# Performance work log

Measured on AMD Instinct MI355X. Metric: run time of the kernel, lower is better.

## Reference

```python
import jax, jax.numpy as jnp
import numpy as np

B, T, I, H, C, S = 512, 128, 512, 512, 97, 26  # batch, enc_len, input, hidden, classes, num_steps


def setup_inputs() -> dict:
    key = jax.random.key(0)
    ks = jax.random.split(key, 12)
    s = 0.05
    d = {}
    d["batch_H"] = jax.random.normal(ks[0], (B, T, I), dtype=jnp.float32)
    d["text"] = jax.random.randint(ks[1], (B, S), 0, C)
    # attention cell params
    d["W_feat"] = jax.random.normal(ks[2], (H, I), dtype=jnp.float32) * s   # feature_projection (no bias)
    d["W_hid"] = jax.random.normal(ks[3], (H, H), dtype=jnp.float32) * s    # hidden_projection
    d["b_hid"] = jnp.zeros((H,), dtype=jnp.float32)
    d["w_score"] = jax.random.normal(ks[4], (H,), dtype=jnp.float32) * s    # attention_score (Linear(H,1), no bias)
    # LSTMCell params, PyTorch gate order [i, f, g, o]
    d["W_ih"] = jax.random.normal(ks[5], (4 * H, I + C), dtype=jnp.float32) * s
    d["W_hh"] = jax.random.normal(ks[6], (4 * H, H), dtype=jnp.float32) * s
    d["b_ih"] = jnp.zeros((4 * H,), dtype=jnp.float32)
    d["b_hh"] = jnp.zeros((4 * H,), dtype=jnp.float32)
    # generator
    d["W_gen"] = jax.random.normal(ks[7], (C, H), dtype=jnp.float32) * s
    d["b_gen"] = jnp.zeros((C,), dtype=jnp.float32)
    return d


def reference(batch_H, text, W_feat, W_hid, b_hid, w_score, W_ih, W_hh, b_ih, b_hh, W_gen, b_gen):
    Bb, Tt, _ = batch_H.shape
    Hh = W_hid.shape[0]
    Cc = W_gen.shape[0]
    # step-invariant: project encoder features once  [B, T, H]
    feat = jnp.einsum('bti,hi->bth', batch_H, W_feat)
    onehots = jax.nn.one_hot(text, Cc, dtype=batch_H.dtype)  # [B, S, C]

    def step(carry, oh):
        h, c = carry
        hp = h @ W_hid.T + b_hid                                     # [B, H]
        e = jnp.einsum('bth,h->bt', jnp.tanh(feat + hp[:, None, :]), w_score)
        alpha = jax.nn.softmax(e, axis=1)                            # [B, T]
        ctx = jnp.einsum('bt,bti->bi', alpha, batch_H)               # [B, I]
        x = jnp.concatenate([ctx, oh], axis=1)                       # [B, I+C]
        gates = x @ W_ih.T + b_ih + h @ W_hh.T + b_hh                # [B, 4H]
        i_g, f_g, g_g, o_g = jnp.split(gates, 4, axis=1)
        c2 = jax.nn.sigmoid(f_g) * c + jax.nn.sigmoid(i_g) * jnp.tanh(g_g)
        h2 = jax.nn.sigmoid(o_g) * jnp.tanh(c2)
        return (h2, c2), h2

    init = (jnp.zeros((Bb, Hh), dtype=batch_H.dtype), jnp.zeros((Bb, Hh), dtype=batch_H.dtype))
    _, hs = jax.lax.scan(step, init, jnp.swapaxes(onehots, 0, 1))    # hs: [S, B, H]
    out_h = jnp.swapaxes(hs, 0, 1)                                   # [B, S, H]
    probs = out_h @ W_gen.T + b_gen                                  # [B, S, C]
    return probs
```

## Files before the change

### kernel.cpp

```cpp
#include <hip/hip_runtime.h>
#include <hip/hip_bf16.h>
#include <stdint.h>
#include <stddef.h>

typedef __bf16 bf16;
typedef __bf16 v8bf __attribute__((ext_vector_type(8)));
typedef float  v4f  __attribute__((ext_vector_type(4)));

#define B_ 512
#define T_ 128
#define I_ 512
#define H_ 512
#define C_ 97
#define S_ 26

__device__ __forceinline__ void async_copy16(void* lds, const void* g) {
  __builtin_amdgcn_global_load_lds((__attribute__((address_space(1))) void*)g,
                                   (__attribute__((address_space(3))) void*)lds,
                                   16, 0, 0);
}

__device__ __forceinline__ float fast_tanh(float x) {
  float e = __expf(2.0f * x);
  return fmaf(-2.0f, __builtin_amdgcn_rcpf(e + 1.0f), 1.0f);
}
__device__ __forceinline__ float fast_sigmoid(float x) {
  float t = __expf(-x);
  return __builtin_amdgcn_rcpf(1.0f + t);
}

__device__ __forceinline__ void zero_acc(v4f acc[4][4]) {
  v4f z = {0.f, 0.f, 0.f, 0.f};
#pragma unroll
  for (int i = 0; i < 4; ++i)
#pragma unroll
    for (int j = 0; j < 4; ++j) acc[i][j] = z;
}

#define WAITBAR(N)                                             \
  do {                                                         \
    asm volatile("s_waitcnt vmcnt(" #N ")" ::: "memory");      \
    __builtin_amdgcn_s_barrier();                              \
    __builtin_amdgcn_sched_barrier(0);                         \
  } while (0)

template <int KTOT>
__device__ __forceinline__ void mm_qb32(const bf16* aRow0, const bf16* aRow1,
                                        const bf16* bRow0, const bf16* bRow1,
                                        bf16* As, bf16* Bs, int tid,
                                        v4f acc[4][4]) {
  constexpr int NT = KTOT / 32;
  const int wave = tid >> 6, lane = tid & 63;
  const int wr = (wave >> 1) * 64, wc = (wave & 1) * 64;
  const int fr = lane & 15, fq = lane >> 4;
  const int s0 = tid * 8;
  const int aB = (wr + fr) * 32 + fq * 8;
  const int bB = (wc + fr) * 32 + fq * 8;
#define STG32(bi, kk)                                   \
  do {                                                  \
    const int o = (bi) * 4096 + s0;                     \
    async_copy16(As + o, aRow0 + (kk));                 \
    async_copy16(As + o + 2048, aRow1 + (kk));          \
    async_copy16(Bs + o, bRow0 + (kk));                 \
    async_copy16(Bs + o + 2048, bRow1 + (kk));          \
  } while (0)
  STG32(0, 0);
  STG32(1, 32);
  for (int t = 0; t < NT; ++t) {
    if (t + 2 < NT) {
      STG32((t + 2) & 3, (t + 2) * 32);
      WAITBAR(8);
    } else if (t + 1 < NT) {
      WAITBAR(4);
    } else {
      WAITBAR(0);
    }
    const int cb = (t & 3) * 4096;
    v8bf av[4], bv[4];
#pragma unroll
    for (int i = 0; i < 4; ++i) av[i] = *(const v8bf*)(As + cb + aB + i * 512);
#pragma unroll
    for (int j = 0; j < 4; ++j) bv[j] = *(const v8bf*)(Bs + cb + bB + j * 512);
#pragma unroll
    for (int i = 0; i < 4; ++i) {
#pragma unroll
      for (int j = 0; j < 4; ++j) {
        acc[i][j] = __builtin_amdgcn_mfma_f32_16x16x32_bf16(av[i], bv[j], acc[i][j], 0, 0, 0);
      }
    }
  }
#undef STG32
}

template <int KTOT>
__device__ __forceinline__ void mm_reg_f32a(const float* aR0, const float* aR1,
                                            const bf16* bRow0, const bf16* bRow1,
                                            bf16* As, bf16* Bs, int tid,
                                            v4f acc[4][4]) {
  const int wave = tid >> 6, lane = tid & 63;
  const int wr = (wave >> 1) * 64, wc = (wave & 1) * 64;
  const int fr = lane & 15, fq = lane >> 4;
  bf16* a_s0 = As + tid * 8;
  bf16* a_s1 = As + (tid + 256) * 8;
  bf16* b_s0 = Bs + tid * 8;
  bf16* b_s1 = Bs + (tid + 256) * 8;
  const bf16* aF[4];
  const bf16* bF[4];
#pragma unroll
  for (int i = 0; i < 4; ++i) {
    aF[i] = As + (wr + i * 16 + fr) * 32 + fq * 8;
    bF[i] = Bs + (wc + i * 16 + fr) * 32 + fq * 8;
  }
  for (int kk = 0; kk < KTOT; kk += 32) {
    v8bf va0, va1;
    const float* p0 = aR0 + kk;
    const float* p1 = aR1 + kk;
    v4f f00 = ((const v4f*)p0)[0], f01 = ((const v4f*)p0)[1];
    v4f f10 = ((const v4f*)p1)[0], f11 = ((const v4f*)p1)[1];
#pragma unroll
    for (int j = 0; j < 4; ++j) {
      va0[j] = (bf16)f00[j]; va0[j + 4] = (bf16)f01[j];
      va1[j] = (bf16)f10[j]; va1[j + 4] = (bf16)f11[j];
    }
    v8bf vb0 = *(const v8bf*)(bRow0 + kk);
    v8bf vb1 = *(const v8bf*)(bRow1 + kk);
    __syncthreads();
    *(v8bf*)a_s0 = va0;
    *(v8bf*)a_s1 = va1;
    *(v8bf*)b_s0 = vb0;
    *(v8bf*)b_s1 = vb1;
    __syncthreads();
    v8bf av[4], bv[4];
#pragma unroll
    for (int i = 0; i < 4; ++i) av[i] = *(const v8bf*)aF[i];
#pragma unroll
    for (int j = 0; j < 4; ++j) bv[j] = *(const v8bf*)bF[j];
#pragma unroll
    for (int i = 0; i < 4; ++i) {
#pragma unroll
      for (int j = 0; j < 4; ++j) {
        acc[i][j] = __builtin_amdgcn_mfma_f32_16x16x32_bf16(av[i], bv[j], acc[i][j], 0, 0, 0);
      }
    }
  }
  __syncthreads();
}

__global__ void k_cvt(const float* __restrict__ src, bf16* __restrict__ dst, int n) {
  int i = (blockIdx.x * 256 + threadIdx.x) * 4;
  if (i + 3 < n) {
    v4f f = *(const v4f*)(src + i);
#pragma unroll
    for (int j = 0; j < 4; ++j) dst[i + j] = (bf16)f[j];
  }
}

__global__ void k_repack(const float* __restrict__ Wih, const float* __restrict__ Whh,
                         bf16* __restrict__ Wcat) {
  int n = blockIdx.x;
  int t = threadIdx.x;
#pragma unroll
  for (int j = 0; j < 4; ++j) {
    int k = t * 4 + j;
    float v = (k < 512) ? Wih[(size_t)n * 609 + k] : Whh[(size_t)n * 512 + (k - 512)];
    Wcat[(size_t)n * 1024 + k] = (bf16)v;
  }
}

__global__ void k_prep_gen(const float* __restrict__ Wg, bf16* __restrict__ Wgen16) {
  int row = blockIdx.x;
  int t = threadIdx.x;
#pragma unroll
  for (int j = 0; j < 2; ++j) {
    int k = t * 2 + j;
    float v = (row < C_) ? Wg[(size_t)row * 512 + k] : 0.0f;
    Wgen16[(size_t)row * 512 + k] = (bf16)v;
  }
}

__global__ void k_prep_oht(const float* __restrict__ Wih, float* __restrict__ OHT) {
  int n = blockIdx.x * 256 + threadIdx.x;
  const float* src = Wih + (size_t)n * 609 + 512;
  for (int c = 0; c < C_; ++c) OHT[(size_t)c * 2048 + n] = src[c];
}


__global__ __launch_bounds__(256, 2) void k_feat16(const bf16* __restrict__ A,
                                                   const bf16* __restrict__ Bw,
                                                   bf16* __restrict__ F) {
  __shared__ bf16 As[4 * 4096];
  __shared__ bf16 Bs[4 * 4096];
  const int tid = threadIdx.x;
  const int m0 = blockIdx.x * 128, n0 = blockIdx.y * 128;
  const int r0 = tid >> 2, k0 = (tid & 3) * 8;
  const bf16* aRow0 = A + (size_t)(m0 + r0) * 512 + k0;
  const bf16* aRow1 = A + (size_t)(m0 + r0 + 64) * 512 + k0;
  const bf16* bRow0 = Bw + (size_t)(n0 + r0) * 512 + k0;
  const bf16* bRow1 = Bw + (size_t)(n0 + r0 + 64) * 512 + k0;
  v4f acc[4][4];
  zero_acc(acc);
  mm_qb32<512>(aRow0, aRow1, bRow0, bRow1, As, Bs, tid, acc);
  const int wave = tid >> 6, lane = tid & 63;
  const int wr = (wave >> 1) * 64, wc = (wave & 1) * 64;
  const int fr = lane & 15, fq = lane >> 4;
#pragma unroll
  for (int i = 0; i < 4; ++i) {
#pragma unroll
    for (int j = 0; j < 4; ++j) {
      int col = n0 + wc + j * 16 + fr;
#pragma unroll
      for (int r = 0; r < 4; ++r) {
        int row = m0 + wr + i * 16 + fq * 4 + r;
        F[(size_t)row * 512 + col] = (bf16)acc[i][j][r];
      }
    }
  }
}

__global__ __launch_bounds__(256, 2) void k_feat32(const float* __restrict__ A,
                                                   const bf16* __restrict__ Bw,
                                                   bf16* __restrict__ F) {
  __shared__ bf16 As[128 * 32];
  __shared__ bf16 Bs[128 * 32];
  const int tid = threadIdx.x;
  const int m0 = blockIdx.x * 128, n0 = blockIdx.y * 128;
  const int r0 = tid >> 2, k0 = (tid & 3) * 8;
  const float* aRow0 = A + (size_t)(m0 + r0) * 512 + k0;
  const float* aRow1 = A + (size_t)(m0 + r0 + 64) * 512 + k0;
  const bf16* bRow0 = Bw + (size_t)(n0 + r0) * 512 + k0;
  const bf16* bRow1 = Bw + (size_t)(n0 + r0 + 64) * 512 + k0;
  v4f acc[4][4];
  zero_acc(acc);
  mm_reg_f32a<512>(aRow0, aRow1, bRow0, bRow1, As, Bs, tid, acc);
  const int wave = tid >> 6, lane = tid & 63;
  const int wr = (wave >> 1) * 64, wc = (wave & 1) * 64;
  const int fr = lane & 15, fq = lane >> 4;
#pragma unroll
  for (int i = 0; i < 4; ++i) {
#pragma unroll
    for (int j = 0; j < 4; ++j) {
      int col = n0 + wc + j * 16 + fr;
#pragma unroll
      for (int r = 0; r < 4; ++r) {
        int row = m0 + wr + i * 16 + fq * 4 + r;
        F[(size_t)row * 512 + col] = (bf16)acc[i][j][r];
      }
    }
  }
}

__global__ __launch_bounds__(256) void k_hp(const bf16* __restrict__ xb_cur,
                                            const bf16* __restrict__ Whid16,
                                            const float* __restrict__ b_hid,
                                            float* __restrict__ P) {
  __shared__ bf16 As[4 * 2048];
  __shared__ bf16 Bs[4 * 4096];
  const int tid = threadIdx.x, wave = tid >> 6, lane = tid & 63;
  const int m0 = blockIdx.x * 32, n0 = blockIdx.y * 64;
  const int fr = lane & 15, fq = lane >> 4;
  const int ra = tid >> 3, sa = (tid & 7) ^ (ra & 7);
  const bf16* aSrc = xb_cur + (size_t)(m0 + ra) * 1024 + 512 + sa * 8;
  const int rb0 = tid >> 3, rb1 = (tid >> 3) + 32;
  const bf16* bSrc0 = Whid16 + (size_t)(n0 + rb0) * 512 + (((tid & 7) ^ (rb0 & 7)) * 8);
  const bf16* bSrc1 = Whid16 + (size_t)(n0 + rb1) * 512 + (((tid & 7) ^ (rb1 & 7)) * 8);
  const int s0 = tid * 8;
  v4f acc[2];
  v4f z = {0.f, 0.f, 0.f, 0.f};
  acc[0] = z; acc[1] = z;
#define STGH(bi, kk)                                    \
  do {                                                  \
    async_copy16(As + (bi) * 2048 + s0, aSrc + (kk));   \
    async_copy16(Bs + (bi) * 4096 + s0, bSrc0 + (kk));  \
    async_copy16(Bs + (bi) * 4096 + 2048 + s0, bSrc1 + (kk)); \
  } while (0)
  STGH(0, 0);
  STGH(1, 64);
  constexpr int NT = 8;
  for (int t = 0; t < NT; ++t) {
    if (t + 2 < NT) {
      STGH((t + 2) & 3, (t + 2) * 64);
      WAITBAR(6);
    } else if (t + 1 < NT) {
      WAITBAR(3);
    } else {
      WAITBAR(0);
    }
    const int cb4 = (t & 3) * 2048;
    const int cb8 = (t & 3) * 4096;
#pragma unroll
    for (int ks = 0; ks < 2; ++ks) {
      const int sw = ((ks * 4 + fq) ^ (fr & 7)) * 8;
      v8bf bv = *(const v8bf*)(Bs + cb8 + (wave * 16 + fr) * 64 + sw);
#pragma unroll
      for (int i = 0; i < 2; ++i) {
        v8bf av = *(const v8bf*)(As + cb4 + (i * 16 + fr) * 64 + sw);
        acc[i] = __builtin_amdgcn_mfma_f32_16x16x32_bf16(av, bv, acc[i], 0, 0, 0);
      }
    }
  }
#undef STGH
  const int col = n0 + wave * 16 + fr;
  const float bh = b_hid[col];
#pragma unroll
  for (int i = 0; i < 2; ++i) {
#pragma unroll
    for (int r = 0; r < 4; ++r) {
      int row = m0 + i * 16 + fq * 4 + r;
      P[(size_t)row * 512 + col] = acc[i][r] + bh;
    }
  }
}

template <bool CTX16>
__global__ __launch_bounds__(512, 4) void k_attn(const bf16* __restrict__ F,
                                                 const float* __restrict__ P,
                                                 const float* __restrict__ w_score,
                                                 const void* __restrict__ bHv,
                                                 bf16* __restrict__ xb_cur) {
  const int b = blockIdx.x;
  const int tid = threadIdx.x, wave = tid >> 6, lane = tid & 63;
  __shared__ float e_s[T_];
  __shared__ float red[8][I_];
  const float CF = 2.8853900817779268f;
  float pl[8], Wv[8];
  {
    const float* p = P + (size_t)b * H_ + lane * 8;
#pragma unroll
    for (int j = 0; j < 8; ++j) pl[j] = CF * p[j];
    const float* w = w_score + lane * 8;
#pragma unroll
    for (int j = 0; j < 8; ++j) Wv[j] = w[j];
  }
  float sW = 0.f;
#pragma unroll
  for (int j = 0; j < 8; ++j) sW += Wv[j];
#pragma unroll
  for (int off = 32; off; off >>= 1) sW += __shfl_xor(sW, off, 64);
  const bf16* Fb = F + (size_t)b * T_ * H_ + lane * 8;
#pragma unroll
  for (int kb = 0; kb < 2; ++kb) {
    v8bf r[8];
#pragma unroll
    for (int u = 0; u < 8; ++u)
      r[u] = *(const v8bf*)(Fb + (size_t)(wave + kb * 64 + u * 8) * H_);
    float a[8];
#pragma unroll
    for (int u = 0; u < 8; ++u) {
      float s = 0.f;
#pragma unroll
      for (int j = 0; j < 8; ++j)
        s = fmaf(Wv[j], __builtin_amdgcn_rcpf(1.0f + exp2f(fmaf(CF, (float)r[u][j], pl[j]))), s);
      a[u] = s;
    }
#pragma unroll
    for (int off = 32; off; off >>= 1) {
#pragma unroll
      for (int u = 0; u < 8; ++u) a[u] += __shfl_xor(a[u], off, 64);
    }
    if (lane == 0) {
#pragma unroll
      for (int u = 0; u < 8; ++u) e_s[wave + kb * 64 + u * 8] = sW - 2.0f * a[u];
    }
  }
  __syncthreads();
  const int i0 = lane * 8;
  float c[8];
#pragma unroll
  for (int j = 0; j < 8; ++j) c[j] = 0.f;
  if (CTX16) {
    const bf16* hb = (const bf16*)bHv + (size_t)b * T_ * I_ + i0;
    v8bf p[8];
#pragma unroll
    for (int u = 0; u < 8; ++u)
      p[u] = *(const v8bf*)(hb + (size_t)(wave + u * 8) * I_);
    float x0, x1;
    {
      float e0 = e_s[lane], e1 = e_s[lane + 64];
      float m = fmaxf(e0, e1);
#pragma unroll
      for (int off = 32; off; off >>= 1) m = fmaxf(m, __shfl_xor(m, off, 64));
      x0 = __expf(e0 - m);
      x1 = __expf(e1 - m);
      float ssum = x0 + x1;
#pragma unroll
      for (int off = 32; off; off >>= 1) ssum += __shfl_xor(ssum, off, 64);
      float inv = __builtin_amdgcn_rcpf(ssum);
      x0 *= inv;
      x1 *= inv;
    }
    float aa[8];
#pragma unroll
    for (int u = 0; u < 8; ++u) aa[u] = __shfl(x0, wave + u * 8, 64);
    v8bf p2[8];
#pragma unroll
    for (int u = 0; u < 8; ++u)
      p2[u] = *(const v8bf*)(hb + (size_t)(64 + wave + u * 8) * I_);
#pragma unroll
    for (int u = 0; u < 8; ++u) {
#pragma unroll
      for (int j = 0; j < 8; ++j) c[j] = fmaf(aa[u], (float)p[u][j], c[j]);
    }
#pragma unroll
    for (int u = 0; u < 8; ++u) aa[u] = __shfl(x1, wave + u * 8, 64);
#pragma unroll
    for (int u = 0; u < 8; ++u) {
#pragma unroll
      for (int j = 0; j < 8; ++j) c[j] = fmaf(aa[u], (float)p2[u][j], c[j]);
    }
  } else {
    float x0, x1;
    {
      float e0 = e_s[lane], e1 = e_s[lane + 64];
      float m = fmaxf(e0, e1);
#pragma unroll
      for (int off = 32; off; off >>= 1) m = fmaxf(m, __shfl_xor(m, off, 64));
      x0 = __expf(e0 - m);
      x1 = __expf(e1 - m);
      float ssum = x0 + x1;
#pragma unroll
      for (int off = 32; off; off >>= 1) ssum += __shfl_xor(ssum, off, 64);
      float inv = __builtin_amdgcn_rcpf(ssum);
      x0 *= inv;
      x1 *= inv;
    }
    const float* hf = (const float*)bHv + (size_t)b * T_ * I_ + i0;
#pragma unroll
    for (int k = 0; k < 4; ++k) {
      const int t = wave + 32 * k;
      float xa = (k < 2) ? x0 : x1;
      float aa0 = __shfl(xa, t & 63, 64);
      float aa1 = __shfl(xa, (t + 8) & 63, 64);
      float aa2 = __shfl(xa, (t + 16) & 63, 64);
      float aa3 = __shfl(xa, (t + 24) & 63, 64);
      const float* p0 = hf + (size_t)t * I_;
      const float* p1 = hf + (size_t)(t + 8) * I_;
      const float* p2 = hf + (size_t)(t + 16) * I_;
      const float* p3 = hf + (size_t)(t + 24) * I_;
      v4f q00 = ((const v4f*)p0)[0], q01 = ((const v4f*)p0)[1];
      v4f q10 = ((const v4f*)p1)[0], q11 = ((const v4f*)p1)[1];
      v4f q20 = ((const v4f*)p2)[0], q21 = ((const v4f*)p2)[1];
      v4f q30 = ((const v4f*)p3)[0], q31 = ((const v4f*)p3)[1];
#pragma unroll
      for (int j = 0; j < 4; ++j) {
        c[j]     = fmaf(aa0, q00[j], c[j]);
        c[j + 4] = fmaf(aa0, q01[j], c[j + 4]);
        c[j]     = fmaf(aa1, q10[j], c[j]);
        c[j + 4] = fmaf(aa1, q11[j], c[j + 4]);
        c[j]     = fmaf(aa2, q20[j], c[j]);
        c[j + 4] = fmaf(aa2, q21[j], c[j + 4]);
        c[j]     = fmaf(aa3, q30[j], c[j]);
        c[j + 4] = fmaf(aa3, q31[j], c[j + 4]);
      }
    }
  }
#pragma unroll
  for (int j = 0; j < 8; ++j) red[wave][i0 + j] = c[j];
  __syncthreads();
  {
    int i = tid;
    float s = red[0][i] + red[1][i] + red[2][i] + red[3][i] +
              red[4][i] + red[5][i] + red[6][i] + red[7][i];
    xb_cur[(size_t)b * 1024 + i] = (bf16)s;
  }
}

__global__ __launch_bounds__(256) void k_gates(const bf16* __restrict__ xb_cur,
                                               const bf16* __restrict__ Wcat,
                                               const float* __restrict__ OHT,
                                               const float* __restrict__ b_ih,
                                               const float* __restrict__ b_hh,
                                               const int* __restrict__ text,
                                               float* __restrict__ c_state,
                                               bf16* __restrict__ out_h,
                                               bf16* __restrict__ xb_nxt, int s) {
  __shared__ union {
    struct { bf16 A[4 * 2048]; bf16 Bv[4 * 8192]; } st;
    float Cs[32 * 132];
  } sm;
  const int tid = threadIdx.x;
  const int m0 = blockIdx.x * 32;
  const int j0 = blockIdx.y * 32;
  const int wave = tid >> 6, lane = tid & 63;
  const int fr = lane & 15, fq = lane >> 4;
  const int s0 = tid * 8;
  const int ra = tid >> 3, sa = (tid & 7) ^ (ra & 7);
  const bf16* aSrc = xb_cur + (size_t)(m0 + ra) * 1024 + sa * 8;
  const bf16* bSrc[4];
#pragma unroll
  for (int cc = 0; cc < 4; ++cc) {
    const int rb = (tid >> 3) + cc * 32;
    const int nw = (rb >> 5) * 512 + j0 + (rb & 31);
    bSrc[cc] = Wcat + (size_t)nw * 1024 + (((tid & 7) ^ (rb & 7)) * 8);
  }
  v4f acc[2][2];
  {
    v4f z = {0.f, 0.f, 0.f, 0.f};
    acc[0][0] = z; acc[0][1] = z; acc[1][0] = z; acc[1][1] = z;
  }
#define STGG(bi, kk)                                                 \
  do {                                                               \
    async_copy16(sm.st.A + (bi) * 2048 + s0, aSrc + (kk));           \
    async_copy16(sm.st.Bv + (bi) * 8192 + s0, bSrc[0] + (kk));       \
    async_copy16(sm.st.Bv + (bi) * 8192 + 2048 + s0, bSrc[1] + (kk)); \
    async_copy16(sm.st.Bv + (bi) * 8192 + 4096 + s0, bSrc[2] + (kk)); \
    async_copy16(sm.st.Bv + (bi) * 8192 + 6144 + s0, bSrc[3] + (kk)); \
  } while (0)
  STGG(0, 0);
  STGG(1, 64);
  constexpr int NT = 16;
  for (int t = 0; t < NT; ++t) {
    if (t + 2 < NT) {
      STGG((t + 2) & 3, (t + 2) * 64);
      WAITBAR(10);
    } else if (t + 1 < NT) {
      WAITBAR(5);
    } else {
      WAITBAR(0);
    }
    const int ca = (t & 3) * 2048;
    const int cbv = (t & 3) * 8192;
#pragma unroll
    for (int ks = 0; ks < 2; ++ks) {
      const int sw = ((ks * 4 + fq) ^ (fr & 7)) * 8;
      v8bf av[2], bv[2];
#pragma unroll
      for (int i = 0; i < 2; ++i)
        av[i] = *(const v8bf*)(sm.st.A + ca + (i * 16 + fr) * 64 + sw);
#pragma unroll
      for (int jf = 0; jf < 2; ++jf)
        bv[jf] = *(const v8bf*)(sm.st.Bv + cbv + (wave * 32 + jf * 16 + fr) * 64 + sw);
#pragma unroll
      for (int i = 0; i < 2; ++i)
#pragma unroll
        for (int jf = 0; jf < 2; ++jf)
          acc[i][jf] = __builtin_amdgcn_mfma_f32_16x16x32_bf16(av[i], bv[jf], acc[i][jf], 0, 0, 0);
    }
  }
#undef STGG
  __syncthreads();
  int tcv[2][4];
#pragma unroll
  for (int i = 0; i < 2; ++i)
#pragma unroll
    for (int r = 0; r < 4; ++r)
      tcv[i][r] = text[(size_t)(m0 + i * 16 + fq * 4 + r) * S_ + s];
#pragma unroll
  for (int jf = 0; jf < 2; ++jf) {
    int cl = wave * 32 + jf * 16 + fr;
    int nw = (cl >> 5) * 512 + j0 + (cl & 31);
    float bias = b_ih[nw] + b_hh[nw];
    const float* oh = OHT + nw;
#pragma unroll
    for (int i = 0; i < 2; ++i) {
#pragma unroll
      for (int r = 0; r < 4; ++r) {
        int rl = i * 16 + fq * 4 + r;
        sm.Cs[rl * 132 + cl] = acc[i][jf][r] + bias + oh[(size_t)tcv[i][r] * 2048];
      }
    }
  }
  __syncthreads();
#pragma unroll
  for (int it = 0; it < 4; ++it) {
    int idx = tid + it * 256;
    int r = idx >> 5, q = idx & 31;
    float ig = sm.Cs[r * 132 + q];
    float fg = sm.Cs[r * 132 + 32 + q];
    float gg = sm.Cs[r * 132 + 64 + q];
    float og = sm.Cs[r * 132 + 96 + q];
    size_t cix = (size_t)(m0 + r) * 512 + j0 + q;
    float c2 = fast_sigmoid(fg) * c_state[cix] + fast_sigmoid(ig) * fast_tanh(gg);
    float h2 = fast_sigmoid(og) * fast_tanh(c2);
    c_state[cix] = c2;
    bf16 hb = (bf16)h2;
    xb_nxt[(size_t)(m0 + r) * 1024 + 512 + j0 + q] = hb;
    out_h[((size_t)(m0 + r) * S_ + s) * 512 + j0 + q] = hb;
  }
}

__global__ __launch_bounds__(256) void k_gen(const bf16* __restrict__ out_h,
                                             const bf16* __restrict__ Wgen16,
                                             const float* __restrict__ b_gen,
                                             float* __restrict__ out) {
  __shared__ bf16 As[4 * 4096];
  __shared__ bf16 Bs[4 * 4096];
  const int tid = threadIdx.x;
  const int m0 = blockIdx.x * 128;
  const int r0 = tid >> 2, k0 = (tid & 3) * 8;
  const bf16* aRow0 = out_h + (size_t)(m0 + r0) * 512 + k0;
  const bf16* aRow1 = out_h + (size_t)(m0 + r0 + 64) * 512 + k0;
  const bf16* bRow0 = Wgen16 + (size_t)r0 * 512 + k0;
  const bf16* bRow1 = Wgen16 + (size_t)(r0 + 64) * 512 + k0;
  v4f acc[4][4];
  zero_acc(acc);
  mm_qb32<512>(aRow0, aRow1, bRow0, bRow1, As, Bs, tid, acc);
  const int wave = tid >> 6, lane = tid & 63;
  const int wr = (wave >> 1) * 64, wc = (wave & 1) * 64;
  const int fr = lane & 15, fq = lane >> 4;
#pragma unroll
  for (int i = 0; i < 4; ++i) {
#pragma unroll
    for (int j = 0; j < 4; ++j) {
      int col = wc + j * 16 + fr;
      if (col < C_) {
        float bg = b_gen[col];
#pragma unroll
        for (int r = 0; r < 4; ++r) {
          int row = m0 + wr + i * 16 + fq * 4 + r;
          out[(size_t)row * C_ + col] = acc[i][j][r] + bg;
        }
      }
    }
  }
}

extern "C" void kernel_launch(void* const* d_in, const int* in_sizes, int n_in,
                              void* d_out, int out_size, void* d_ws, size_t ws_size,
                              hipStream_t stream) {
  (void)in_sizes; (void)n_in; (void)out_size;
  const float* batch_H = (const float*)d_in[0];
  const int*   text    = (const int*)d_in[1];
  const float* W_feat  = (const float*)d_in[2];
  const float* W_hid   = (const float*)d_in[3];
  const float* b_hid   = (const float*)d_in[4];
  const float* w_score = (const float*)d_in[5];
  const float* W_ih    = (const float*)d_in[6];
  const float* W_hh    = (const float*)d_in[7];
  const float* b_ih    = (const float*)d_in[8];
  const float* b_hh    = (const float*)d_in[9];
  const float* W_gen   = (const float*)d_in[10];
  const float* b_gen   = (const float*)d_in[11];
  float* out = (float*)d_out;

  char* ws = (char*)d_ws;
  bf16*  F       = (bf16*)(ws);
  bf16*  out_h   = (bf16*)(ws + 67108864);
  float* P       = (float*)(ws + 80740352);
  bf16*  xb0     = (bf16*)(ws + 81788928);
  bf16*  xb1     = (bf16*)(ws + 82837504);
  float* c_state = (float*)(ws + 83886080);
  bf16*  Wcat    = (bf16*)(ws + 84934656);
  bf16*  Wf16    = (bf16*)(ws + 89128960);
  bf16*  Whid16  = (bf16*)(ws + 89653248);
  bf16*  Wgen16  = (bf16*)(ws + 90177536);
  float* OHT     = (float*)(ws + 90308608);
  bf16*  bH16    = (bf16*)(ws + 91357184);
  const bool useBH16 = (ws_size >= (size_t)158466048);

  bf16* xb[2] = {xb0, xb1};

  hipMemsetAsync(xb0, 0, (size_t)512 * 1024 * 2, stream);
  hipMemsetAsync(c_state, 0, (size_t)512 * 512 * 4, stream);

  k_cvt<<<dim3(256), 256, 0, stream>>>(W_feat, Wf16, 512 * 512);
  k_cvt<<<dim3(256), 256, 0, stream>>>(W_hid, Whid16, 512 * 512);
  k_repack<<<dim3(2048), 256, 0, stream>>>(W_ih, W_hh, Wcat);
  k_prep_gen<<<dim3(128), 256, 0, stream>>>(W_gen, Wgen16);
  k_prep_oht<<<dim3(8), 256, 0, stream>>>(W_ih, OHT);

  if (useBH16) {
    k_cvt<<<dim3(32768), 256, 0, stream>>>(batch_H, bH16, B_ * T_ * I_);
    k_feat16<<<dim3(512, 4), 256, 0, stream>>>(bH16, Wf16, F);
  } else {
    k_feat32<<<dim3(512, 4), 256, 0, stream>>>(batch_H, Wf16, F);
  }

  for (int s = 0; s < S_; ++s) {
    bf16* cur = xb[s & 1];
    bf16* nxt = xb[(s + 1) & 1];
    k_hp<<<dim3(16, 8), 256, 0, stream>>>(cur, Whid16, b_hid, P);
    if (useBH16) {
      k_attn<true><<<dim3(512), 512, 0, stream>>>(F, P, w_score, bH16, cur);
    } else {
      k_attn<false><<<dim3(512), 512, 0, stream>>>(F, P, w_score, batch_H, cur);
    }
    k_gates<<<dim3(16, 16), 256, 0, stream>>>(cur, Wcat, OHT, b_ih, b_hh, text,
                                              c_state, out_h, nxt, s);
  }
  k_gen<<<dim3(104, 1), 256, 0, stream>>>(out_h, Wgen16, b_gen, out);
}
```

Measured before the change: 1.451 ms.

## Fuse prep kernels, add MFMA priority hints, remap grids for XCD locality

Merges the six weight and input conversion kernels into one launch to cut launch overhead. Wraps the MFMA loops in feat16, k_hp and k_gates with s_setprio so matrix issue gets scheduling priority. It also flattens the k_hp and k_gates grids and remaps block indices so each XCD (blockIdx mod 8) handles a contiguous set of weight columns, aiming at better L2 reuse of weights. The index remaps are meant to keep coverage identical, and the fused prep kernel relies on branching by block range.

```diff
diff --git a/kernel.cpp b/kernel.cpp
--- a/kernel.cpp
+++ b/kernel.cpp
@@ -81,6 +81,7 @@
     for (int i = 0; i < 4; ++i) av[i] = *(const v8bf*)(As + cb + aB + i * 512);
 #pragma unroll
     for (int j = 0; j < 4; ++j) bv[j] = *(const v8bf*)(Bs + cb + bB + j * 512);
+    __builtin_amdgcn_s_setprio(1);
 #pragma unroll
     for (int i = 0; i < 4; ++i) {
 #pragma unroll
@@ -88,6 +89,7 @@
         acc[i][j] = __builtin_amdgcn_mfma_f32_16x16x32_bf16(av[i], bv[j], acc[i][j], 0, 0, 0);
       }
     }
+    __builtin_amdgcn_s_setprio(0);
   }
 #undef STG32
 }
@@ -146,42 +148,54 @@
   __syncthreads();
 }
 
-__global__ void k_cvt(const float* __restrict__ src, bf16* __restrict__ dst, int n) {
-  int i = (blockIdx.x * 256 + threadIdx.x) * 4;
-  if (i + 3 < n) {
-    v4f f = *(const v4f*)(src + i);
-#pragma unroll
-    for (int j = 0; j < 4; ++j) dst[i + j] = (bf16)f[j];
-  }
-}
-
-__global__ void k_repack(const float* __restrict__ Wih, const float* __restrict__ Whh,
-                         bf16* __restrict__ Wcat) {
-  int n = blockIdx.x;
-  int t = threadIdx.x;
-#pragma unroll
-  for (int j = 0; j < 4; ++j) {
-    int k = t * 4 + j;
-    float v = (k < 512) ? Wih[(size_t)n * 609 + k] : Whh[(size_t)n * 512 + (k - 512)];
-    Wcat[(size_t)n * 1024 + k] = (bf16)v;
-  }
-}
-
-__global__ void k_prep_gen(const float* __restrict__ Wg, bf16* __restrict__ Wgen16) {
-  int row = blockIdx.x;
-  int t = threadIdx.x;
-#pragma unroll
-  for (int j = 0; j < 2; ++j) {
-    int k = t * 2 + j;
-    float v = (row < C_) ? Wg[(size_t)row * 512 + k] : 0.0f;
-    Wgen16[(size_t)row * 512 + k] = (bf16)v;
-  }
-}
-
-__global__ void k_prep_oht(const float* __restrict__ Wih, float* __restrict__ OHT) {
-  int n = blockIdx.x * 256 + threadIdx.x;
-  const float* src = Wih + (size_t)n * 609 + 512;
-  for (int c = 0; c < C_; ++c) OHT[(size_t)c * 2048 + n] = src[c];
+__global__ void k_prep_all(const float* __restrict__ batch_H, bf16* __restrict__ bH16, int nbh,
+                           const float* __restrict__ W_feat, bf16* __restrict__ Wf16,
+                           const float* __restrict__ W_hid, bf16* __restrict__ Whid16,
+                           const float* __restrict__ Wih, const float* __restrict__ Whh,
+                           bf16* __restrict__ Wcat,
+                           const float* __restrict__ Wg, bf16* __restrict__ Wgen16,
+                           float* __restrict__ OHT) {
+  int b = blockIdx.x;
+  const int t = threadIdx.x;
+  if (b < nbh) {
+    int i = (b * 256 + t) * 4;
+    v4f f = *(const v4f*)(batch_H + i);
+#pragma unroll
+    for (int j = 0; j < 4; ++j) bH16[i + j] = (bf16)f[j];
+    return;
+  }
+  b -= nbh;
+  if (b < 256) {
+    int i = (b * 256 + t) * 4;
+    v4f f = *(const v4f*)(W_feat + i);
+#pragma unroll
+    for (int j = 0; j < 4; ++j) Wf16[i + j] = (bf16)f[j];
+  } else if (b < 512) {
+    int i = ((b - 256) * 256 + t) * 4;
+    v4f f = *(const v4f*)(W_hid + i);
+#pragma unroll
+    for (int j = 0; j < 4; ++j) Whid16[i + j] = (bf16)f[j];
+  } else if (b < 2560) {
+    int n = b - 512;
+#pragma unroll
+    for (int j = 0; j < 4; ++j) {
+      int k = t * 4 + j;
+      float v = (k < 512) ? Wih[(size_t)n * 609 + k] : Whh[(size_t)n * 512 + (k - 512)];
+      Wcat[(size_t)n * 1024 + k] = (bf16)v;
+    }
+  } else if (b < 2688) {
+    int row = b - 2560;
+#pragma unroll
+    for (int j = 0; j < 2; ++j) {
+      int k = t * 2 + j;
+      float v = (row < C_) ? Wg[(size_t)row * 512 + k] : 0.0f;
+      Wgen16[(size_t)row * 512 + k] = (bf16)v;
+    }
+  } else {
+    int n = (b - 2688) * 256 + t;
+    const float* src = Wih + (size_t)n * 609 + 512;
+    for (int c = 0; c < C_; ++c) OHT[(size_t)c * 2048 + n] = src[c];
+  }
 }
 
 
@@ -256,7 +270,9 @@
   __shared__ bf16 As[4 * 2048];
   __shared__ bf16 Bs[4 * 4096];
   const int tid = threadIdx.x, wave = tid >> 6, lane = tid & 63;
-  const int m0 = blockIdx.x * 32, n0 = blockIdx.y * 64;
+  const int flat = blockIdx.x;
+  const int m0 = (flat >> 3) * 32;
+  const int n0 = (flat & 7) * 64;
   const int fr = lane & 15, fq = lane >> 4;
   const int ra = tid >> 3, sa = (tid & 7) ^ (ra & 7);
   const bf16* aSrc = xb_cur + (size_t)(m0 + ra) * 1024 + 512 + sa * 8;
@@ -291,11 +307,13 @@
     for (int ks = 0; ks < 2; ++ks) {
       const int sw = ((ks * 4 + fq) ^ (fr & 7)) * 8;
       v8bf bv = *(const v8bf*)(Bs + cb8 + (wave * 16 + fr) * 64 + sw);
+      __builtin_amdgcn_s_setprio(1);
 #pragma unroll
       for (int i = 0; i < 2; ++i) {
         v8bf av = *(const v8bf*)(As + cb4 + (i * 16 + fr) * 64 + sw);
         acc[i] = __builtin_amdgcn_mfma_f32_16x16x32_bf16(av, bv, acc[i], 0, 0, 0);
       }
+      __builtin_amdgcn_s_setprio(0);
     }
   }
 #undef STGH
@@ -478,8 +496,11 @@
     float Cs[32 * 132];
   } sm;
   const int tid = threadIdx.x;
-  const int m0 = blockIdx.x * 32;
-  const int j0 = blockIdx.y * 32;
+  const int flat = blockIdx.x;
+  const int xcd = flat & 7;
+  const int idx = flat >> 3;
+  const int m0 = (idx >> 1) * 32;
+  const int j0 = (xcd * 2 + (idx & 1)) * 32;
   const int wave = tid >> 6, lane = tid & 63;
   const int fr = lane & 15, fq = lane >> 4;
   const int s0 = tid * 8;
@@ -529,11 +550,13 @@
 #pragma unroll
       for (int jf = 0; jf < 2; ++jf)
         bv[jf] = *(const v8bf*)(sm.st.Bv + cbv + (wave * 32 + jf * 16 + fr) * 64 + sw);
+      __builtin_amdgcn_s_setprio(1);
 #pragma unroll
       for (int i = 0; i < 2; ++i)
 #pragma unroll
         for (int jf = 0; jf < 2; ++jf)
           acc[i][jf] = __builtin_amdgcn_mfma_f32_16x16x32_bf16(av[i], bv[jf], acc[i][jf], 0, 0, 0);
+      __builtin_amdgcn_s_setprio(0);
     }
   }
 #undef STGG
@@ -562,8 +585,8 @@
   __syncthreads();
 #pragma unroll
   for (int it = 0; it < 4; ++it) {
-    int idx = tid + it * 256;
-    int r = idx >> 5, q = idx & 31;
+    int idx2 = tid + it * 256;
+    int r = idx2 >> 5, q = idx2 & 31;
     float ig = sm.Cs[r * 132 + q];
     float fg = sm.Cs[r * 132 + 32 + q];
     float gg = sm.Cs[r * 132 + 64 + q];
@@ -652,14 +675,12 @@
   hipMemsetAsync(xb0, 0, (size_t)512 * 1024 * 2, stream);
   hipMemsetAsync(c_state, 0, (size_t)512 * 512 * 4, stream);
 
-  k_cvt<<<dim3(256), 256, 0, stream>>>(W_feat, Wf16, 512 * 512);
-  k_cvt<<<dim3(256), 256, 0, stream>>>(W_hid, Whid16, 512 * 512);
-  k_repack<<<dim3(2048), 256, 0, stream>>>(W_ih, W_hh, Wcat);
-  k_prep_gen<<<dim3(128), 256, 0, stream>>>(W_gen, Wgen16);
-  k_prep_oht<<<dim3(8), 256, 0, stream>>>(W_ih, OHT);
+  const int nbh = useBH16 ? 32768 : 0;
+  k_prep_all<<<dim3(nbh + 2696), 256, 0, stream>>>(
+      batch_H, bH16, nbh, W_feat, Wf16, W_hid, Whid16,
+      W_ih, W_hh, Wcat, W_gen, Wgen16, OHT);
 
   if (useBH16) {
-    k_cvt<<<dim3(32768), 256, 0, stream>>>(batch_H, bH16, B_ * T_ * I_);
     k_feat16<<<dim3(512, 4), 256, 0, stream>>>(bH16, Wf16, F);
   } else {
     k_feat32<<<dim3(512, 4), 256, 0, stream>>>(batch_H, Wf16, F);
@@ -668,14 +689,14 @@
   for (int s = 0; s < S_; ++s) {
     bf16* cur = xb[s & 1];
     bf16* nxt = xb[(s + 1) & 1];
-    k_hp<<<dim3(16, 8), 256, 0, stream>>>(cur, Whid16, b_hid, P);
+    k_hp<<<dim3(128), 256, 0, stream>>>(cur, Whid16, b_hid, P);
     if (useBH16) {
       k_attn<true><<<dim3(512), 512, 0, stream>>>(F, P, w_score, bH16, cur);
     } else {
       k_attn<false><<<dim3(512), 512, 0, stream>>>(F, P, w_score, batch_H, cur);
     }
-    k_gates<<<dim3(16, 16), 256, 0, stream>>>(cur, Wcat, OHT, b_ih, b_hh, text,
-                                              c_state, out_h, nxt, s);
+    k_gates<<<dim3(256), 256, 0, stream>>>(cur, Wcat, OHT, b_ih, b_hh, text,
+                                           c_state, out_h, nxt, s);
   }
   k_gen<<<dim3(104, 1), 256, 0, stream>>>(out_h, Wgen16, b_gen, out);
 }
```

Result: no change. 1.441 ms (-0.7%).
